# Optimization experiments

Hardware: AMD Instinct MI355X
Metric: run time of the kernel (lower is better)

The kernel has to match this reference:

```python
import jax, jax.numpy as jnp
import numpy as np

TEMPERATURE = 0.07
N_CLASSES = 100


def setup_inputs() -> dict:
    key = jax.random.key(0)
    k1, k2 = jax.random.split(key)
    N, D = 8192, 128
    emb = jax.random.normal(k1, (N, D), dtype=jnp.float32)
    # unit-normalize so exp(sim / temperature) stays finite in fp32
    emb = emb / jnp.linalg.norm(emb, axis=1, keepdims=True)
    labels = jax.random.randint(k2, (N,), 0, N_CLASSES, dtype=jnp.int64)
    return {"embeddings": emb, "labels": labels}


def reference(embeddings, labels):
    N = embeddings.shape[0]
    dt = embeddings.dtype
    # [N, N] similarity
    sim = jnp.matmul(embeddings, embeddings.T) / TEMPERATURE
    off_diag = 1.0 - jnp.eye(N, dtype=dt)
    pos_mask = (labels[:, None] == labels[None, :]).astype(dt) * off_diag
    exp_sim = jnp.exp(sim) * off_diag  # diagonal zeroed
    positive_sum = jnp.sum(exp_sim * pos_mask, axis=1)
    total_sum = jnp.sum(exp_sim, axis=1)
    loss = -jnp.log(positive_sum / (total_sum + 1e-8) + 1e-8)
    valid = pos_mask.sum(axis=1) > 0
    cnt = jnp.sum(valid.astype(dt))
    mean_loss = jnp.where(
        cnt > 0,
        jnp.sum(jnp.where(valid, loss, jnp.zeros_like(loss))) / jnp.maximum(cnt, 1.0),
        jnp.asarray(0.0, dtype=dt),
    )
    return mean_loss
```

## Files before the change

### kernel.cpp

```cpp
#include <hip/hip_runtime.h>

#define N 8192
#define D 128

using short8  = __attribute__((ext_vector_type(8))) short;
using float4v = __attribute__((ext_vector_type(4))) float;

static __device__ inline unsigned int f2bf(float f) {
    union { float f; unsigned int u; } x;
    x.f = f;
    unsigned int u = x.u;
    return (u + 0x7FFFu + ((u >> 16) & 1u)) >> 16;
}

__global__ __launch_bounds__(256, 2) void cl_main(
    const float* __restrict__ emb, const int* __restrict__ labels,
    float* __restrict__ tot, float* __restrict__ pos)
{
    __shared__ uint4 ldsB[128 * 16];

    const int tid  = threadIdx.x;
    const int lane = tid & 63;
    const int wave = tid >> 6;
    const int q    = lane >> 4;
    const int c    = lane & 15;
    const int rb   = blockIdx.x * 128;
    const int rw   = rb + wave * 32;

    short8 afrag[2][4];
    int rowlab[2][4];
    #pragma unroll
    for (int tr = 0; tr < 2; ++tr) {
        const int arow = rw + tr * 16 + c;
        #pragma unroll
        for (int ks = 0; ks < 4; ++ks) {
            const float* p = emb + arow * D + ks * 32 + q * 8;
            float4v f0 = *(const float4v*)p;
            float4v f1 = *(const float4v*)(p + 4);
            short8 a;
            a[0] = (short)f2bf(f0[0]); a[1] = (short)f2bf(f0[1]);
            a[2] = (short)f2bf(f0[2]); a[3] = (short)f2bf(f0[3]);
            a[4] = (short)f2bf(f1[0]); a[5] = (short)f2bf(f1[1]);
            a[6] = (short)f2bf(f1[2]); a[7] = (short)f2bf(f1[3]);
            afrag[tr][ks] = a;
        }
        #pragma unroll
        for (int reg = 0; reg < 4; ++reg)
            rowlab[tr][reg] = labels[rw + tr * 16 + q * 4 + reg];
    }

    float tot_a[2][4] = {{0.f,0.f,0.f,0.f},{0.f,0.f,0.f,0.f}};
    float pos_a[2][4] = {{0.f,0.f,0.f,0.f},{0.f,0.f,0.f,0.f}};
    const float invT = 1.0f / 0.07f;

    for (int it = 0; it < 8; ++it) {
        const int cbase = blockIdx.y * 1024 + it * 128;

        #pragma unroll
        for (int i = 0; i < 8; ++i) {
            const int g     = tid + i * 256;
            const int brow  = g >> 4;
            const int chunk = g & 15;
            const float* p = emb + (cbase + brow) * D + chunk * 8;
            float4v f0 = *(const float4v*)p;
            float4v f1 = *(const float4v*)(p + 4);
            uint4 u;
            u.x = f2bf(f0[0]) | (f2bf(f0[1]) << 16);
            u.y = f2bf(f0[2]) | (f2bf(f0[3]) << 16);
            u.z = f2bf(f1[0]) | (f2bf(f1[1]) << 16);
            u.w = f2bf(f1[2]) | (f2bf(f1[3]) << 16);
            ldsB[brow * 16 + (chunk ^ (brow & 15))] = u;
        }
        int collab[8];
        #pragma unroll
        for (int tc = 0; tc < 8; ++tc) collab[tc] = labels[cbase + tc * 16 + c];
        __syncthreads();

        float4v acc[2][8];
        #pragma unroll
        for (int tr = 0; tr < 2; ++tr)
            #pragma unroll
            for (int tc = 0; tc < 8; ++tc) {
                float4v z = {0.f, 0.f, 0.f, 0.f};
                acc[tr][tc] = z;
            }

        const short8* ldsS = (const short8*)ldsB;
        #pragma unroll
        for (int ks = 0; ks < 4; ++ks) {
            short8 bfr[8];
            #pragma unroll
            for (int tc = 0; tc < 8; ++tc) {
                const int brow  = tc * 16 + c;
                const int chunk = ks * 4 + q;
                bfr[tc] = ldsS[brow * 16 + (chunk ^ (brow & 15))];
            }
            #pragma unroll
            for (int tr = 0; tr < 2; ++tr)
                #pragma unroll
                for (int tc = 0; tc < 8; ++tc)
                    acc[tr][tc] = __builtin_amdgcn_mfma_f32_16x16x32_bf16(
                        afrag[tr][ks], bfr[tc], acc[tr][tc], 0, 0, 0);
        }

        #pragma unroll
        for (int tr = 0; tr < 2; ++tr) {
            const int rtile = rw + tr * 16;
            #pragma unroll
            for (int tc = 0; tc < 8; ++tc) {
                const bool diag_tile = (rtile == cbase + tc * 16);
                const int lc = collab[tc];
                #pragma unroll
                for (int reg = 0; reg < 4; ++reg) {
                    float v = __expf(acc[tr][tc][reg] * invT);
                    if (diag_tile && (q * 4 + reg) == c) v = 0.f;
                    tot_a[tr][reg] += v;
                    if (rowlab[tr][reg] == lc) pos_a[tr][reg] += v;
                }
            }
        }
        __syncthreads();
    }

    #pragma unroll
    for (int tr = 0; tr < 2; ++tr)
        #pragma unroll
        for (int reg = 0; reg < 4; ++reg) {
            float t = tot_a[tr][reg];
            float p = pos_a[tr][reg];
            #pragma unroll
            for (int m = 1; m < 16; m <<= 1) {
                t += __shfl_xor(t, m, 64);
                p += __shfl_xor(p, m, 64);
            }
            if (c == 0) {
                const int r = rw + tr * 16 + q * 4 + reg;
                atomicAdd(&tot[r], t);
                atomicAdd(&pos[r], p);
            }
        }
}

__global__ void cl_finalize(const int* __restrict__ labels,
                            const float* __restrict__ tot,
                            const float* __restrict__ pos,
                            float* __restrict__ out)
{
    __shared__ int hist[128];
    __shared__ float ssum[4], scnt[4];
    const int tid = threadIdx.x;
    if (tid < 128) hist[tid] = 0;
    __syncthreads();
    for (int i = tid; i < N; i += 256) atomicAdd(&hist[labels[i] & 127], 1);
    __syncthreads();

    float lsum = 0.f, lcnt = 0.f;
    for (int i = tid; i < N; i += 256) {
        const int cc = hist[labels[i] & 127] - 1;
        const float loss = -__logf(pos[i] / (tot[i] + 1e-8f) + 1e-8f);
        if (cc > 0) { lsum += loss; lcnt += 1.f; }
    }
    #pragma unroll
    for (int m = 1; m < 64; m <<= 1) {
        lsum += __shfl_xor(lsum, m, 64);
        lcnt += __shfl_xor(lcnt, m, 64);
    }
    const int wave = tid >> 6;
    if ((tid & 63) == 0) { ssum[wave] = lsum; scnt[wave] = lcnt; }
    __syncthreads();
    if (tid == 0) {
        const float s = ssum[0] + ssum[1] + ssum[2] + ssum[3];
        const float n = scnt[0] + scnt[1] + scnt[2] + scnt[3];
        out[0] = (n > 0.f) ? s / fmaxf(n, 1.f) : 0.f;
    }
}

extern "C" void kernel_launch(void* const* d_in, const int* in_sizes, int n_in,
                              void* d_out, int out_size, void* d_ws, size_t ws_size,
                              hipStream_t stream) {
    const float* emb   = (const float*)d_in[0];
    const int* labels  = (const int*)d_in[1];
    float* tot = (float*)d_ws;
    float* pos = tot + N;

    hipMemsetAsync(d_ws, 0, 2 * N * sizeof(float), stream);
    cl_main<<<dim3(64, 8), 256, 0, stream>>>(emb, labels, tot, pos);
    cl_finalize<<<1, 256, 0, stream>>>(labels, tot, pos, (float*)d_out);
}
```

Baseline: 112.7 us.

## Fuse finalize into main kernel via last-block ticket and double grid

Removes the separate finalize kernel launch: each block takes an atomic ticket and the last block computes the mean loss from the accumulated row sums. Grid width over columns doubles (16 column slices of 512) with each block doing half the iterations, and launch bounds rise to 4 blocks per SM for more occupancy. The MFMA loop interleaves B fragment loads with MFMAs to cut register pressure. The validity test changes from a label histogram to pos>0, which differs only if every same-label exp value underflows to zero; the extra threadfence and ticket serialization add a small tail cost.

```diff
diff --git a/kernel.cpp b/kernel.cpp
--- a/kernel.cpp
+++ b/kernel.cpp
@@ -13,19 +13,21 @@
     return (u + 0x7FFFu + ((u >> 16) & 1u)) >> 16;
 }
 
-__global__ __launch_bounds__(256, 2) void cl_main(
+__global__ __launch_bounds__(256, 4) void cl_main(
     const float* __restrict__ emb, const int* __restrict__ labels,
-    float* __restrict__ tot, float* __restrict__ pos)
+    float* __restrict__ tot, float* __restrict__ pos,
+    int* __restrict__ ticket, float* __restrict__ out)
 {
     __shared__ uint4 ldsB[128 * 16];
+    __shared__ float sred[2][4];
+    __shared__ int s_ticket;
 
     const int tid  = threadIdx.x;
     const int lane = tid & 63;
     const int wave = tid >> 6;
     const int q    = lane >> 4;
     const int c    = lane & 15;
-    const int rb   = blockIdx.x * 128;
-    const int rw   = rb + wave * 32;
+    const int rw   = blockIdx.x * 128 + wave * 32;
 
     short8 afrag[2][4];
     int rowlab[2][4];
@@ -53,8 +55,8 @@
     float pos_a[2][4] = {{0.f,0.f,0.f,0.f},{0.f,0.f,0.f,0.f}};
     const float invT = 1.0f / 0.07f;
 
-    for (int it = 0; it < 8; ++it) {
-        const int cbase = blockIdx.y * 1024 + it * 128;
+    for (int it = 0; it < 4; ++it) {
+        const int cbase = blockIdx.y * 512 + it * 128;
 
         #pragma unroll
         for (int i = 0; i < 8; ++i) {
@@ -88,19 +90,16 @@
         const short8* ldsS = (const short8*)ldsB;
         #pragma unroll
         for (int ks = 0; ks < 4; ++ks) {
-            short8 bfr[8];
             #pragma unroll
             for (int tc = 0; tc < 8; ++tc) {
                 const int brow  = tc * 16 + c;
                 const int chunk = ks * 4 + q;
-                bfr[tc] = ldsS[brow * 16 + (chunk ^ (brow & 15))];
+                short8 b = ldsS[brow * 16 + (chunk ^ (brow & 15))];
+                #pragma unroll
+                for (int tr = 0; tr < 2; ++tr)
+                    acc[tr][tc] = __builtin_amdgcn_mfma_f32_16x16x32_bf16(
+                        afrag[tr][ks], b, acc[tr][tc], 0, 0, 0);
             }
-            #pragma unroll
-            for (int tr = 0; tr < 2; ++tr)
-                #pragma unroll
-                for (int tc = 0; tc < 8; ++tc)
-                    acc[tr][tc] = __builtin_amdgcn_mfma_f32_16x16x32_bf16(
-                        afrag[tr][ks], bfr[tc], acc[tr][tc], 0, 0, 0);
         }
 
         #pragma unroll
@@ -139,38 +138,35 @@
                 atomicAdd(&pos[r], p);
             }
         }
-}
 
-__global__ void cl_finalize(const int* __restrict__ labels,
-                            const float* __restrict__ tot,
-                            const float* __restrict__ pos,
-                            float* __restrict__ out)
-{
-    __shared__ int hist[128];
-    __shared__ float ssum[4], scnt[4];
-    const int tid = threadIdx.x;
-    if (tid < 128) hist[tid] = 0;
+    __threadfence();
     __syncthreads();
-    for (int i = tid; i < N; i += 256) atomicAdd(&hist[labels[i] & 127], 1);
+    if (tid == 0)
+        s_ticket = __hip_atomic_fetch_add(ticket, 1, __ATOMIC_ACQ_REL,
+                                          __HIP_MEMORY_SCOPE_AGENT);
     __syncthreads();
+    if (s_ticket != 64 * 16 - 1) return;
 
+    __threadfence();
     float lsum = 0.f, lcnt = 0.f;
     for (int i = tid; i < N; i += 256) {
-        const int cc = hist[labels[i] & 127] - 1;
-        const float loss = -__logf(pos[i] / (tot[i] + 1e-8f) + 1e-8f);
-        if (cc > 0) { lsum += loss; lcnt += 1.f; }
+        const float t = __hip_atomic_load(&tot[i], __ATOMIC_RELAXED,
+                                          __HIP_MEMORY_SCOPE_AGENT);
+        const float p = __hip_atomic_load(&pos[i], __ATOMIC_RELAXED,
+                                          __HIP_MEMORY_SCOPE_AGENT);
+        const float loss = -__logf(p / (t + 1e-8f) + 1e-8f);
+        if (p > 0.f) { lsum += loss; lcnt += 1.f; }
     }
     #pragma unroll
     for (int m = 1; m < 64; m <<= 1) {
         lsum += __shfl_xor(lsum, m, 64);
         lcnt += __shfl_xor(lcnt, m, 64);
     }
-    const int wave = tid >> 6;
-    if ((tid & 63) == 0) { ssum[wave] = lsum; scnt[wave] = lcnt; }
+    if (lane == 0) { sred[0][wave] = lsum; sred[1][wave] = lcnt; }
     __syncthreads();
     if (tid == 0) {
-        const float s = ssum[0] + ssum[1] + ssum[2] + ssum[3];
-        const float n = scnt[0] + scnt[1] + scnt[2] + scnt[3];
+        const float s = sred[0][0] + sred[0][1] + sred[0][2] + sred[0][3];
+        const float n = sred[1][0] + sred[1][1] + sred[1][2] + sred[1][3];
         out[0] = (n > 0.f) ? s / fmaxf(n, 1.f) : 0.f;
     }
 }
@@ -180,10 +176,11 @@
                               hipStream_t stream) {
     const float* emb   = (const float*)d_in[0];
     const int* labels  = (const int*)d_in[1];
-    float* tot = (float*)d_ws;
-    float* pos = tot + N;
+    float* tot    = (float*)d_ws;
+    float* pos    = tot + N;
+    int*   ticket = (int*)(pos + N);
 
-    hipMemsetAsync(d_ws, 0, 2 * N * sizeof(float), stream);
-    cl_main<<<dim3(64, 8), 256, 0, stream>>>(emb, labels, tot, pos);
-    cl_finalize<<<1, 256, 0, stream>>>(labels, tot, pos, (float*)d_out);
+    hipMemsetAsync(d_ws, 0, (2 * N + 1) * sizeof(float), stream);
+    cl_main<<<dim3(64, 16), 256, 0, stream>>>(emb, labels, tot, pos, ticket,
+                                              (float*)d_out);
 }
```

After: 274.9 us. +143.8%, slower.
